# Kernel tuning notes

Hardware: AMD Instinct MI355X
Metric: run time of the kernel (lower is better)

Reference implementation:

```python
import jax, jax.numpy as jnp
import numpy as np

B, T, M, E, H = 8, 1024, 8192, 1024, 128
DECAY = 0.01
LQ_ADD = 1e-4
POS_TABLE_SIZE = 32


def setup_inputs() -> dict:
    key = jax.random.key(0)
    ks = jax.random.split(key, 9)
    return {
        "block_pos_list": jax.random.randint(ks[0], (B,), 0, 10),
        "inp": jax.random.normal(ks[1], (B, T, E), jnp.float32),
        "memory": jax.random.normal(ks[2], (B, M, E), jnp.float32),
        "memory_block_dist": jax.random.randint(ks[3], (B, M), 0, 1000).astype(jnp.int32),
        "memory_rank": jax.random.normal(ks[4], (B, M), jnp.float32),
        "pos_table": jax.random.normal(ks[5], (POS_TABLE_SIZE, E), jnp.float32) * 0.02,
        "Wk": jax.random.normal(ks[6], (H, E), jnp.float32) / np.float32(np.sqrt(E)),
        "Wq": jax.random.normal(ks[7], (H, E), jnp.float32) / np.float32(np.sqrt(E)),
        "Wv": jax.random.normal(ks[8], (H, E), jnp.float32) / np.float32(np.sqrt(E)),
    }


def reference(block_pos_list, inp, memory, memory_block_dist, memory_rank, pos_table, Wk, Wq, Wv):
    # --- reset slots where block_pos == 0 (start of a new work) ---
    reset = (block_pos_list == 0)                               # [B]
    memory = jnp.where(reset[:, None, None], 0.0, memory)       # [B, M, E]
    dist = jnp.where(reset[:, None], 0, memory_block_dist) + 1  # [B, M]

    # --- log2-bucketed positional embedding added to memory ---
    m_pos_ix = jnp.floor(jnp.log2(dist.astype(jnp.float32))).astype(jnp.int32)
    m_with_emb = memory + pos_table[m_pos_ix]                   # [B, M, E]
    mk = jnp.concatenate([m_with_emb, inp], axis=1)             # [B, M+T, E]

    # --- projections (torch Linear: x @ W.T) ---
    k = jnp.einsum('bse,he->bsh', mk, Wk)                       # [B, M+T, H]
    q = jnp.einsum('bte,he->bth', inp, Wq)                      # [B, T, H]
    v = jnp.einsum('bse,he->bsh', mk, Wv)                       # [B, M+T, H]

    # --- square + max-normalize attention (not softmax) ---
    mbs = M + T
    wei = jnp.einsum('bth,bsh->bts', q, k) * np.float32(mbs ** -0.5)  # [B, T, M+T]
    wei = wei * wei
    wei = wei / jnp.max(wei, axis=2, keepdims=True)

    # --- per-slot rank update ---
    mean_wei = jnp.mean(jnp.sum(wei, axis=1), axis=1)           # [B]
    new_rank = memory_rank + jnp.sum(wei[:, :, :M], axis=1) / mean_wei[:, None] - 1.0 - DECAY

    # --- sort memory slots by rank (descending), evict bottom block ---
    order = jnp.argsort(-new_rank, axis=1)                      # [B, M]
    mem_s = jnp.take_along_axis(memory, order[:, :, None], axis=1)
    dist_s = jnp.take_along_axis(dist, order, axis=1)
    rank_s = jnp.take_along_axis(new_rank, order, axis=1)
    r = min(T, M)
    new_memory = jax.lax.stop_gradient(mem_s.at[:, -r:].set(inp[:, -r:]))
    new_dist = dist_s.at[:, -r:].set(0)
    new_rank_out = jax.lax.stop_gradient(rank_s.at[:, -r:].set(1.0))

    qt_loss = jnp.sum(jnp.log(wei + LQ_ADD))
    out = jnp.einsum('bts,bsh->bth', wei, v)                    # [B, T, H]
    return out, qt_loss, new_memory, new_dist, new_rank_out
```

## Files before the change

### kernel.cpp

```cpp
#include <hip/hip_runtime.h>
#include <hip/hip_bf16.h>
#include <stdint.h>

#define BB 8
#define TT 1024
#define MM 8192
#define EE 1024
#define HH 128
#define SS (MM + TT)
#define RKEEP (MM - 1024)
#define NSPLIT 8
#define SCHUNK (SS / NSPLIT)
#define NT (SCHUNK / 64)
#define BK 32

typedef __attribute__((ext_vector_type(8))) short bf16x8;
typedef __attribute__((ext_vector_type(4))) short s16x4;
typedef __attribute__((ext_vector_type(4))) float f32x4;

static __device__ __forceinline__ unsigned f2ord(float f) {
    unsigned u = __float_as_uint(f);
    return u ^ ((u & 0x80000000u) ? 0xFFFFFFFFu : 0x80000000u);
}
static __device__ __forceinline__ float ord2f(unsigned o) {
    unsigned u = (o & 0x80000000u) ? (o ^ 0x80000000u) : ~o;
    return __uint_as_float(u);
}
static __device__ __forceinline__ unsigned short f2bf(float x) {
    unsigned u = __float_as_uint(x);
    unsigned r = u + 0x7FFFu + ((u >> 16) & 1u);
    return (unsigned short)(r >> 16);
}

static __device__ __forceinline__ void gload_lds16(const short* g, short* l) {
    __builtin_amdgcn_global_load_lds(
        (const __attribute__((address_space(1))) void*)g,
        (__attribute__((address_space(3))) void*)l, 16, 0, 0);
}

__device__ const float SCALEF = (float)(1.0 / 96.0);

__global__ __launch_bounds__(256) void k_wsplit(
    const float* __restrict__ Wk, const float* __restrict__ Wq, const float* __restrict__ Wv,
    short* __restrict__ wk, short* __restrict__ wq, short* __restrict__ wv)
{
    int idx = blockIdx.x * 256 + threadIdx.x;
    int m = idx >> 15;
    int o4 = (idx & 32767) * 4;
    const float* W = m == 0 ? Wk : (m == 1 ? Wq : Wv);
    short* D = m == 0 ? wk : (m == 1 ? wq : wv);
    f32x4 v = *(const f32x4*)&W[o4];
    s16x4 h;
#pragma unroll
    for (int j = 0; j < 4; ++j) h[j] = (short)f2bf(v[j]);
    *(s16x4*)&D[o4] = h;
}

__global__ __launch_bounds__(256, 4) void k_proj_kv(
    const float* __restrict__ memory, const int* __restrict__ mbd,
    const int* __restrict__ bpl, const float* __restrict__ pos_table,
    const float* __restrict__ inp,
    const short* __restrict__ wk, const short* __restrict__ wv,
    short* __restrict__ kb, short* __restrict__ vT)
{
    __shared__ __align__(16) short smA[64 * 64];
    __shared__ __align__(16) short smB[2][2][128 * 32];

    const int tid = threadIdx.x;
    const int b   = blockIdx.y;
    const int s0  = blockIdx.x * 64;
    const bool reset = (bpl[b] == 0);
    const int lane = tid & 63, wid = tid >> 6;
    const int wc = wid;
    const int fr = lane & 15, fq = lane >> 4;

    const int arow = tid >> 2;
    const int aq   = tid & 3;
    int pix;
    const float* abase;
    {
        int s = s0 + arow;
        if (s < MM) {
            int d = reset ? 1 : (mbd[b * MM + s] + 1);
            pix = 31 - __clz(d);
            abase = reset ? nullptr : &memory[((size_t)b * MM + s) * EE];
        } else {
            pix = -1;
            abase = &inp[((size_t)b * TT + (s - MM)) * EE];
        }
    }

    f32x4 accK[4][2], accV[4][2];
#pragma unroll
    for (int m = 0; m < 4; ++m)
#pragma unroll
        for (int n = 0; n < 2; ++n) {
            accK[m][n] = (f32x4){0.f, 0.f, 0.f, 0.f};
            accV[m][n] = (f32x4){0.f, 0.f, 0.f, 0.f};
        }

    const int wh   = (tid >> 2);
    const int wk8  = (tid & 3) * 8;
    const int wdst = wid * 512;

    auto STAGEW = [&](int e0, int buf) {
#pragma unroll
        for (int p = 0; p < 2; ++p) {
            int h = p * 64 + wh;
            int ec = wk8 ^ ((h & 3) << 3);
            size_t g = (size_t)h * EE + e0 + ec;
            gload_lds16(&wk[g], &smB[buf][0][p * 2048 + wdst]);
            gload_lds16(&wv[g], &smB[buf][1][p * 2048 + wdst]);
        }
    };
    auto LOADP = [&](int p, f32x4 xa[4]) {
        int e0 = p * 64 + aq * 16;
#pragma unroll
        for (int j = 0; j < 4; ++j) {
            f32x4 v = (f32x4){0.f, 0.f, 0.f, 0.f};
            if (abase) v = *(const f32x4*)&abase[e0 + j * 4];
            if (pix >= 0) {
                f32x4 pt = *(const f32x4*)&pos_table[(size_t)pix * EE + e0 + j * 4];
                v[0] += pt[0]; v[1] += pt[1]; v[2] += pt[2]; v[3] += pt[3];
            }
            xa[j] = v;
        }
    };
    auto STOREP = [&](const f32x4 xa[4]) {
#pragma unroll
        for (int j = 0; j < 2; ++j) {
            bf16x8 h;
#pragma unroll
            for (int c = 0; c < 4; ++c) {
                h[c]     = (short)f2bf(xa[2 * j][c]);
                h[4 + c] = (short)f2bf(xa[2 * j + 1][c]);
            }
            int g = (aq * 2 + j) ^ (arow & 7);
            *(bf16x8*)&smA[arow * 64 + g * 8] = h;
        }
    };

    f32x4 xa[4];
    LOADP(0, xa);
    STOREP(xa);
    STAGEW(0, 0);
    __syncthreads();
    LOADP(1, xa);

    for (int step = 0; step < 32; ++step) {
        const int wbuf = step & 1;
        const int sseg = step & 1;
        if (step < 31) STAGEW((step + 1) * BK, wbuf ^ 1);

        bf16x8 ah[4];
#pragma unroll
        for (int m = 0; m < 4; ++m) {
            int r = m * 16 + fr;
            int g = (sseg * 4 + fq) ^ (r & 7);
            ah[m] = *(const bf16x8*)&smA[r * 64 + g * 8];
        }
#pragma unroll
        for (int n = 0; n < 2; ++n) {
            int c = wc * 32 + n * 16 + fr;
            int off = c * 32 + ((fq * 8) ^ ((c & 3) << 3));
            bf16x8 kh = *(const bf16x8*)&smB[wbuf][0][off];
            bf16x8 vh = *(const bf16x8*)&smB[wbuf][1][off];
#pragma unroll
            for (int m = 0; m < 4; ++m) {
                accK[m][n] = __builtin_amdgcn_mfma_f32_16x16x32_bf16(ah[m], kh, accK[m][n], 0, 0, 0);
                accV[m][n] = __builtin_amdgcn_mfma_f32_16x16x32_bf16(ah[m], vh, accV[m][n], 0, 0, 0);
            }
        }
        __syncthreads();
        if (sseg == 1 && step < 31) {
            STOREP(xa);
            __syncthreads();
            if (step < 29) LOADP((step >> 1) + 2, xa);
        }
    }

#pragma unroll
    for (int m = 0; m < 4; ++m) {
        int row = s0 + m * 16 + fq * 4;
#pragma unroll
        for (int n = 0; n < 2; ++n) {
            int col = wc * 32 + n * 16 + fr;
#pragma unroll
            for (int i = 0; i < 4; ++i)
                kb[((size_t)b * SS + row + i) * HH + col] = (short)f2bf(accK[m][n][i]);
        }
    }
    float* tpT = (float*)smB;
#pragma unroll
    for (int hp = 0; hp < 4; ++hp) {
        __syncthreads();
        if (wc == hp) {
#pragma unroll
            for (int m = 0; m < 4; ++m)
#pragma unroll
                for (int n = 0; n < 2; ++n) {
                    int cl = n * 16 + fr;
                    int row = m * 16 + fq * 4;
                    *(f32x4*)&tpT[cl * 68 + row] = accV[m][n];
                }
        }
        __syncthreads();
        for (int idx = tid; idx < 32 * 16; idx += 256) {
            int hcl = idx >> 4, s4 = (idx & 15) << 2;
            f32x4 v = *(const f32x4*)&tpT[hcl * 68 + s4];
            s16x4 hi;
#pragma unroll
            for (int j = 0; j < 4; ++j) hi[j] = (short)f2bf(v[j]);
            size_t o = ((size_t)b * HH + hp * 32 + hcl) * SS + s0 + s4;
            *(s16x4*)&vT[o] = hi;
        }
    }
}

__global__ __launch_bounds__(256, 4) void k_proj_q(
    const float* __restrict__ inp, const short* __restrict__ wq,
    short* __restrict__ qb)
{
    __shared__ __align__(16) short smA[64 * 64];
    __shared__ __align__(16) short smB[2][128 * 32];
    const int tid = threadIdx.x;
    const int b   = blockIdx.y;
    const int t0  = blockIdx.x * 64;
    const int lane = tid & 63, wid = tid >> 6;
    const int wc = wid;
    const int fr = lane & 15, fq = lane >> 4;
    const int arow = tid >> 2, aq = tid & 3;
    const int wh   = (tid >> 2);
    const int wk8  = (tid & 3) * 8;
    const int wdst = wid * 512;
    const float* abase = &inp[((size_t)b * TT + t0 + arow) * EE];

    f32x4 acc[4][2];
#pragma unroll
    for (int m = 0; m < 4; ++m)
#pragma unroll
        for (int n = 0; n < 2; ++n) acc[m][n] = (f32x4){0.f, 0.f, 0.f, 0.f};

    auto STAGEWQ = [&](int e0, int buf) {
#pragma unroll
        for (int p = 0; p < 2; ++p) {
            int h = p * 64 + wh;
            int ec = wk8 ^ ((h & 3) << 3);
            size_t g = (size_t)h * EE + e0 + ec;
            gload_lds16(&wq[g], &smB[buf][p * 2048 + wdst]);
        }
    };
    auto LOADP = [&](int p, f32x4 xa[4]) {
        int e0 = p * 64 + aq * 16;
#pragma unroll
        for (int j = 0; j < 4; ++j) xa[j] = *(const f32x4*)&abase[e0 + j * 4];
    };
    auto STOREP = [&](const f32x4 xa[4]) {
#pragma unroll
        for (int j = 0; j < 2; ++j) {
            bf16x8 h;
#pragma unroll
            for (int c = 0; c < 4; ++c) {
                h[c]     = (short)f2bf(xa[2 * j][c]);
                h[4 + c] = (short)f2bf(xa[2 * j + 1][c]);
            }
            int g = (aq * 2 + j) ^ (arow & 7);
            *(bf16x8*)&smA[arow * 64 + g * 8] = h;
        }
    };

    f32x4 xa[4];
    LOADP(0, xa);
    STOREP(xa);
    STAGEWQ(0, 0);
    __syncthreads();
    LOADP(1, xa);

    for (int step = 0; step < 32; ++step) {
        const int wbuf = step & 1;
        const int sseg = step & 1;
        if (step < 31) STAGEWQ((step + 1) * BK, wbuf ^ 1);

        bf16x8 ah[4];
#pragma unroll
        for (int m = 0; m < 4; ++m) {
            int r = m * 16 + fr;
            int g = (sseg * 4 + fq) ^ (r & 7);
            ah[m] = *(const bf16x8*)&smA[r * 64 + g * 8];
        }
#pragma unroll
        for (int n = 0; n < 2; ++n) {
            int c = wc * 32 + n * 16 + fr;
            int off = c * 32 + ((fq * 8) ^ ((c & 3) << 3));
            bf16x8 bh = *(const bf16x8*)&smB[wbuf][off];
#pragma unroll
            for (int m = 0; m < 4; ++m)
                acc[m][n] = __builtin_amdgcn_mfma_f32_16x16x32_bf16(ah[m], bh, acc[m][n], 0, 0, 0);
        }
        __syncthreads();
        if (sseg == 1 && step < 31) {
            STOREP(xa);
            __syncthreads();
            if (step < 29) LOADP((step >> 1) + 2, xa);
        }
    }
#pragma unroll
    for (int m = 0; m < 4; ++m) {
        int row = t0 + m * 16 + fq * 4;
#pragma unroll
        for (int n = 0; n < 2; ++n) {
            int col = wc * 32 + n * 16 + fr;
#pragma unroll
            for (int i = 0; i < 4; ++i)
                qb[((size_t)b * TT + row + i) * HH + col] = (short)f2bf(acc[m][n][i]);
        }
    }
}

__device__ __forceinline__ void stage_k64_async(const short* __restrict__ src,
                                                size_t rowBase, int tid, short* sh)
{
#pragma unroll
    for (int c2 = 0; c2 < 4; ++c2) {
        int srow = c2 * 16 + (tid >> 4);
        int scol = ((tid & 15) * 8) ^ ((srow & 7) << 3);
        size_t g = (rowBase + srow) * HH + scol;
        gload_lds16(&src[g], &sh[c2 * 2048 + (tid >> 6) * 512]);
    }
}

__device__ __forceinline__ void stage_v64_async(const short* __restrict__ vT,
                                                int b, int st, int tid, short* vs)
{
#pragma unroll
    for (int c2 = 0; c2 < 4; ++c2) {
        int h = c2 * 32 + (tid >> 3);
        int sc = ((tid & 7) * 8) ^ ((h & 7) << 3);
        size_t g = ((size_t)b * HH + h) * SS + st + sc;
        gload_lds16(&vT[g], &vs[c2 * 2048 + (tid >> 6) * 512]);
    }
}

__device__ __forceinline__ void load_qfrags(const short* __restrict__ qb,
                                            size_t rowIx, int fq, bf16x8 qh[4])
{
    size_t base = rowIx * HH + fq * 8;
#pragma unroll
    for (int k = 0; k < 4; ++k)
        qh[k] = *(const bf16x8*)&qb[base + k * 32];
}

__device__ __forceinline__ void qk_mfma4(const bf16x8 qh[4], const short* sh,
                                         int fr, int fq, f32x4 acc[4])
{
#pragma unroll
    for (int n = 0; n < 4; ++n) {
        int sc = n * 16 + fr;
        int ro = sc * 128, msk = (sc & 7) << 3;
#pragma unroll
        for (int k = 0; k < 4; ++k) {
            int off = ro + ((k * 32 + fq * 8) ^ msk);
            bf16x8 bh = *(const bf16x8*)&sh[off];
            acc[n] = __builtin_amdgcn_mfma_f32_16x16x32_bf16(qh[k], bh, acc[n], 0, 0, 0);
        }
    }
}

__global__ __launch_bounds__(256) void k_rowmax(
    const short* __restrict__ qb, const short* __restrict__ kb,
    float* __restrict__ rowmax)
{
    __shared__ short Ks[2][64 * 128];
    const int tid = threadIdx.x, lane = tid & 63, wloc = tid >> 6;
    const int fr = lane & 15, fq = lane >> 4;
    const int split = blockIdx.x, t0 = blockIdx.y * 64, b = blockIdx.z;

    bf16x8 qh[4];
    load_qfrags(qb, (size_t)b * TT + t0 + wloc * 16 + fr, fq, qh);

    float rm[4] = {0.f, 0.f, 0.f, 0.f};
    const int sBeg = split * SCHUNK;
    const size_t kbase = (size_t)b * SS;

    stage_k64_async(kb, kbase + sBeg, tid, Ks[0]);
    __syncthreads();
    for (int t = 0; t < NT; ++t) {
        const int bf = t & 1;
        if (t + 1 < NT)
            stage_k64_async(kb, kbase + sBeg + (t + 1) * 64, tid, Ks[bf ^ 1]);
        f32x4 acc[4];
#pragma unroll
        for (int n = 0; n < 4; ++n) acc[n] = (f32x4){0.f, 0.f, 0.f, 0.f};
        qk_mfma4(qh, Ks[bf], fr, fq, acc);
#pragma unroll
        for (int n = 0; n < 4; ++n)
#pragma unroll
            for (int i = 0; i < 4; ++i) {
                float w = acc[n][i] * SCALEF;
                rm[i] = fmaxf(rm[i], w * w);
            }
        __syncthreads();
    }
#pragma unroll
    for (int d = 1; d < 16; d <<= 1)
#pragma unroll
        for (int i = 0; i < 4; ++i)
            rm[i] = fmaxf(rm[i], __shfl_xor(rm[i], d, 64));
    if (fr == 0)
#pragma unroll
        for (int i = 0; i < 4; ++i)
            atomicMax((int*)&rowmax[b * TT + t0 + wloc * 16 + fq * 4 + i], __float_as_int(rm[i]));
}

__global__ __launch_bounds__(256) void k_attn(
    const short* __restrict__ qb, const short* __restrict__ kb,
    const short* __restrict__ vT,
    const float* __restrict__ rowmax,
    float* __restrict__ outAcc, float* __restrict__ cpart, float* __restrict__ qtloss)
{
    __shared__ short Ks[2][64 * 128];
    __shared__ short Vs[2][128 * 64];
    __shared__ short Ph[64 * 64];
    __shared__ float csLDS[SCHUNK];
    __shared__ float qred[256];
    const int tid = threadIdx.x, lane = tid & 63, wloc = tid >> 6;
    const int fr = lane & 15, fq = lane >> 4;
    const int split = blockIdx.x, t0 = blockIdx.y * 64, b = blockIdx.z;

    for (int i = tid; i < SCHUNK; i += 256) csLDS[i] = 0.f;

    bf16x8 qh[4];
    load_qfrags(qb, (size_t)b * TT + t0 + wloc * 16 + fr, fq, qh);

    float inv[4];
#pragma unroll
    for (int i = 0; i < 4; ++i)
        inv[i] = 1.0f / rowmax[b * TT + t0 + wloc * 16 + fq * 4 + i];

    f32x4 oacc[8];
#pragma unroll
    for (int n = 0; n < 8; ++n) oacc[n] = (f32x4){0.f, 0.f, 0.f, 0.f};
    float qtp = 0.f;

    const int sBeg = split * SCHUNK;
    const size_t kbase = (size_t)b * SS;

    stage_k64_async(kb, kbase + sBeg, tid, Ks[0]);
    stage_v64_async(vT, b, sBeg, tid, Vs[0]);

    for (int t = 0; t < NT; ++t) {
        const int bf = t & 1;
        __syncthreads();

        f32x4 acc[4];
#pragma unroll
        for (int n = 0; n < 4; ++n) acc[n] = (f32x4){0.f, 0.f, 0.f, 0.f};
        qk_mfma4(qh, Ks[bf], fr, fq, acc);

#pragma unroll
        for (int n = 0; n < 4; ++n) {
            float cp = 0.f;
#pragma unroll
            for (int i = 0; i < 4; ++i) {
                float w = acc[n][i] * SCALEF;
                float w2 = w * w;
                float wei = w2 * inv[i];
                qtp += __logf(wei + 1e-4f);
                cp += wei;
                int r = wloc * 16 + fq * 4 + i;
                int sw = (n * 16 + fr) ^ ((r & 7) << 3);
                Ph[r * 64 + sw] = (short)f2bf(wei);
            }
            cp += __shfl_xor(cp, 16, 64);
            cp += __shfl_xor(cp, 32, 64);
            if (fq == 0) atomicAdd(&csLDS[t * 64 + n * 16 + fr], cp);
        }
        __syncthreads();
        if (t + 1 < NT) {
            stage_k64_async(kb, kbase + sBeg + (t + 1) * 64, tid, Ks[bf ^ 1]);
            stage_v64_async(vT, b, sBeg + (t + 1) * 64, tid, Vs[bf ^ 1]);
        }
        {
            int rA = wloc * 16 + fr;
#pragma unroll
            for (int k = 0; k < 2; ++k) {
                int offA = rA * 64 + ((k * 32 + fq * 8) ^ ((rA & 7) << 3));
                bf16x8 ph = *(const bf16x8*)&Ph[offA];
#pragma unroll
                for (int n = 0; n < 8; ++n) {
                    int hc = n * 16 + fr;
                    int offB = hc * 64 + ((k * 32 + fq * 8) ^ ((hc & 7) << 3));
                    bf16x8 vh = *(const bf16x8*)&Vs[bf][offB];
                    oacc[n] = __builtin_amdgcn_mfma_f32_16x16x32_bf16(ph, vh, oacc[n], 0, 0, 0);
                }
            }
        }
    }

#pragma unroll
    for (int n = 0; n < 8; ++n)
#pragma unroll
        for (int i = 0; i < 4; ++i)
            atomicAdd(&outAcc[((size_t)b * TT + t0 + wloc * 16 + fq * 4 + i) * HH + n * 16 + fr],
                      oacc[n][i]);

    qred[tid] = qtp;
    __syncthreads();
    for (int off = 128; off; off >>= 1) {
        if (tid < off) qred[tid] += qred[tid + off];
        __syncthreads();
    }
    if (tid == 0) atomicAdd(qtloss, qred[0]);

    const int tt = blockIdx.y;
    for (int s = tid; s < SCHUNK; s += 256)
        cpart[((size_t)(b * 16 + tt)) * SS + sBeg + s] = csLDS[s];
}

__global__ __launch_bounds__(256) void k_rank(
    const float* __restrict__ cpart, const float* __restrict__ mrank,
    unsigned long long* __restrict__ keys, float* __restrict__ csum)
{
    const int b = blockIdx.x, tid = threadIdx.x;
    __shared__ float red[256];
    float p = 0.f;
    for (int s = tid; s < SS; s += 256) {
        float cs = 0.f;
#pragma unroll
        for (int tt = 0; tt < 16; ++tt) cs += cpart[((size_t)(b * 16 + tt)) * SS + s];
        csum[b * SS + s] = cs;
        p += cs;
    }
    red[tid] = p;
    __syncthreads();
    for (int off = 128; off; off >>= 1) {
        if (tid < off) red[tid] += red[tid + off];
        __syncthreads();
    }
    float mean = red[0] / (float)SS;
    for (int m = tid; m < MM; m += 256) {
        float rank = ((mrank[b * MM + m] + csum[b * SS + m] / mean) - 1.0f) - 0.01f;
        keys[b * MM + m] = ((unsigned long long)(unsigned)(~f2ord(rank)) << 32) | (unsigned)m;
    }
}

__global__ __launch_bounds__(1024) void k_sort(unsigned long long* __restrict__ keys)
{
    __shared__ unsigned long long a[MM];
    const int b = blockIdx.x, tid = threadIdx.x;
    for (int i = tid; i < MM; i += 1024) a[i] = keys[(size_t)b * MM + i];
    __syncthreads();
    for (int k = 2; k <= MM; k <<= 1) {
        for (int j = k >> 1; j > 0; j >>= 1) {
            for (int i = tid; i < MM; i += 1024) {
                int l = i ^ j;
                if (l > i) {
                    unsigned long long x = a[i], y = a[l];
                    bool up = ((i & k) == 0);
                    if ((x > y) == up) { a[i] = y; a[l] = x; }
                }
            }
            __syncthreads();
        }
    }
    for (int i = tid; i < MM; i += 1024) keys[(size_t)b * MM + i] = a[i];
}

__global__ __launch_bounds__(256) void k_scatter(
    const float* __restrict__ memory, const int* __restrict__ mbd,
    const int* __restrict__ bpl, const float* __restrict__ inp,
    const unsigned long long* __restrict__ keys,
    float* __restrict__ nmem, float* __restrict__ ndist, float* __restrict__ nrank)
{
    const int blk = blockIdx.x;
    const int b = blk >> 10;
    const int p0 = (blk & 1023) * 8;
    const bool reset = (bpl[b] == 0);
    const int tid = threadIdx.x;
    const f32x4 zero = (f32x4){0.f, 0.f, 0.f, 0.f};

    f32x4 vr[8];
    float dist[8], rankv[8];
#pragma unroll
    for (int r = 0; r < 8; ++r) {
        int p = p0 + r;
        if (p < RKEEP) {
            unsigned long long key = keys[(size_t)b * MM + p];
            int src = (int)(unsigned)(key & 0xFFFFFFFFu);
            vr[r] = reset ? zero
                          : *(const f32x4*)&memory[((size_t)b * MM + src) * EE + tid * 4];
            dist[r]  = reset ? 1.0f : (float)(mbd[b * MM + src] + 1);
            rankv[r] = ord2f(~(unsigned)(key >> 32));
        } else {
            int irow = p - RKEEP;
            vr[r] = *(const f32x4*)&inp[((size_t)b * TT + irow) * EE + tid * 4];
            dist[r] = 0.f; rankv[r] = 1.0f;
        }
    }
#pragma unroll
    for (int r = 0; r < 8; ++r) {
        int p = p0 + r;
        *(f32x4*)&nmem[((size_t)b * MM + p) * EE + tid * 4] = vr[r];
        if (tid == 0) { ndist[b * MM + p] = dist[r]; nrank[b * MM + p] = rankv[r]; }
    }
}

extern "C" void kernel_launch(void* const* d_in, const int* in_sizes, int n_in,
                              void* d_out, int out_size, void* d_ws, size_t ws_size,
                              hipStream_t stream)
{
    const int*   bpl    = (const int*)d_in[0];
    const float* inp    = (const float*)d_in[1];
    const float* memory = (const float*)d_in[2];
    const int*   mbd    = (const int*)d_in[3];
    const float* mrank  = (const float*)d_in[4];
    const float* pos    = (const float*)d_in[5];
    const float* Wk     = (const float*)d_in[6];
    const float* Wq     = (const float*)d_in[7];
    const float* Wv     = (const float*)d_in[8];

    float* out   = (float*)d_out;
    float* qtl   = out + (size_t)BB * TT * HH;
    float* nmem  = qtl + 1;
    float* ndist = nmem + (size_t)BB * MM * EE;
    float* nrank = ndist + (size_t)BB * MM;

    char* w = (char*)d_ws;
    short* qb = (short*)w; w += (size_t)BB * TT * HH * 2;
    short* kb = (short*)w; w += (size_t)BB * SS * HH * 2;
    short* vT = (short*)w; w += (size_t)BB * HH * SS * 2;
    float* rmax = (float*)w; w += (size_t)BB * TT * 4;
    float* csum = (float*)w; w += (size_t)BB * SS * 4;
    float* cpart = (float*)w; w += (size_t)BB * 16 * SS * 4;
    unsigned long long* keys = (unsigned long long*)w; w += (size_t)BB * MM * 8;
    short* wk = (short*)w; w += (size_t)HH * EE * 2;
    short* wq = (short*)w; w += (size_t)HH * EE * 2;
    short* wv = (short*)w; w += (size_t)HH * EE * 2;
    if ((size_t)(w - (char*)d_ws) > ws_size) return;

    hipMemsetAsync(d_out, 0, ((size_t)BB * TT * HH + 1) * 4, stream);
    hipMemsetAsync(rmax, 0, (size_t)BB * TT * 4, stream);

    k_wsplit <<<384, 256, 0, stream>>>(Wk, Wq, Wv, wk, wq, wv);
    k_proj_kv<<<dim3(SS / 64, BB), 256, 0, stream>>>(memory, mbd, bpl, pos, inp,
                                                     wk, wv, kb, vT);
    k_proj_q <<<dim3(TT / 64, BB), 256, 0, stream>>>(inp, wq, qb);
    k_rowmax <<<dim3(NSPLIT, TT / 64, BB), 256, 0, stream>>>(qb, kb, rmax);
    k_attn   <<<dim3(NSPLIT, TT / 64, BB), 256, 0, stream>>>(qb, kb, vT,
                                                             rmax, out, cpart, qtl);
    k_rank   <<<BB, 256, 0, stream>>>(cpart, mrank, keys, csum);
    k_sort   <<<BB, 1024, 0, stream>>>(keys);
    k_scatter<<<BB * (MM / 8), 256, 0, stream>>>(memory, mbd, bpl, inp, keys, nmem, ndist, nrank);
}
```

Measured before the change: 575.4 us.

## Deepen async load pipelines with explicit vmcnt waits and raw barriers

Replaces __syncthreads in the projection GEMM loops with explicit s_waitcnt vmcnt/lgkmcnt plus s_barrier, and double-buffers the fp32 activation prefetch registers so global loads run two phases ahead. The rowmax kernel moves to a triple-buffered K tile with one barrier per iteration, and the attention kernel issues the next K/V tile loads before computing on the current tile instead of after. The aim is to hide global-load latency and cut barrier stalls. The cost is more registers and LDS, and hand-tuned wait counts that must exactly match the number of outstanding loads per thread, or reads could race.

```diff
diff --git a/kernel.cpp b/kernel.cpp
--- a/kernel.cpp
+++ b/kernel.cpp
@@ -17,6 +17,11 @@
 typedef __attribute__((ext_vector_type(8))) short bf16x8;
 typedef __attribute__((ext_vector_type(4))) short s16x4;
 typedef __attribute__((ext_vector_type(4))) float f32x4;
+
+#define VMCNT(n) asm volatile("s_waitcnt vmcnt(" #n ")" ::: "memory")
+#define LGKM0()  asm volatile("s_waitcnt lgkmcnt(0)" ::: "memory")
+#define SBAR()   __builtin_amdgcn_s_barrier()
+#define SCB()    __builtin_amdgcn_sched_barrier(0)
 
 static __device__ __forceinline__ unsigned f2ord(float f) {
     unsigned u = __float_as_uint(f);
@@ -118,11 +123,14 @@
 #pragma unroll
         for (int j = 0; j < 4; ++j) {
             f32x4 v = (f32x4){0.f, 0.f, 0.f, 0.f};
-            if (abase) v = *(const f32x4*)&abase[e0 + j * 4];
             if (pix >= 0) {
                 f32x4 pt = *(const f32x4*)&pos_table[(size_t)pix * EE + e0 + j * 4];
                 v[0] += pt[0]; v[1] += pt[1]; v[2] += pt[2]; v[3] += pt[3];
             }
+            if (abase) {
+                f32x4 mv = *(const f32x4*)&abase[e0 + j * 4];
+                v[0] += mv[0]; v[1] += mv[1]; v[2] += mv[2]; v[3] += mv[3];
+            }
             xa[j] = v;
         }
     };
@@ -140,18 +148,23 @@
         }
     };
 
-    f32x4 xa[4];
-    LOADP(0, xa);
-    STOREP(xa);
+    f32x4 xaA[4], xaB[4];
+    LOADP(0, xaA);
+    STOREP(xaA);
     STAGEW(0, 0);
     __syncthreads();
-    LOADP(1, xa);
+    LOADP(1, xaB);
+    LOADP(2, xaA);
 
     for (int step = 0; step < 32; ++step) {
         const int wbuf = step & 1;
+        if (step < 31) STAGEW((step + 1) * BK, wbuf ^ 1);
+        if (step == 31)                      { VMCNT(0); }
+        else if ((step & 1) || step >= 28)   { VMCNT(4); }
+        else                                 { VMCNT(8); }
+        SCB(); SBAR(); SCB();
+
         const int sseg = step & 1;
-        if (step < 31) STAGEW((step + 1) * BK, wbuf ^ 1);
-
         bf16x8 ah[4];
 #pragma unroll
         for (int m = 0; m < 4; ++m) {
@@ -171,11 +184,17 @@
                 accV[m][n] = __builtin_amdgcn_mfma_f32_16x16x32_bf16(ah[m], vh, accV[m][n], 0, 0, 0);
             }
         }
-        __syncthreads();
-        if (sseg == 1 && step < 31) {
-            STOREP(xa);
-            __syncthreads();
-            if (step < 29) LOADP((step >> 1) + 2, xa);
+
+        if (step < 31) {
+            SCB(); SBAR(); SCB();
+            if (step & 1) {
+                if ((step & 2) == 0) STOREP(xaB); else STOREP(xaA);
+                LGKM0(); SCB(); SBAR(); SCB();
+                if (step <= 25) {
+                    int np = (step >> 1) + 3;
+                    if ((step & 2) == 0) LOADP(np, xaB); else LOADP(np, xaA);
+                }
+            }
         }
     }
 
@@ -269,18 +288,23 @@
         }
     };
 
-    f32x4 xa[4];
-    LOADP(0, xa);
-    STOREP(xa);
+    f32x4 xaA[4], xaB[4];
+    LOADP(0, xaA);
+    STOREP(xaA);
     STAGEWQ(0, 0);
     __syncthreads();
-    LOADP(1, xa);
+    LOADP(1, xaB);
+    LOADP(2, xaA);
 
     for (int step = 0; step < 32; ++step) {
         const int wbuf = step & 1;
+        if (step < 31) STAGEWQ((step + 1) * BK, wbuf ^ 1);
+        if (step == 31)                      { VMCNT(0); }
+        else if ((step & 1) || step >= 28)   { VMCNT(4); }
+        else                                 { VMCNT(8); }
+        SCB(); SBAR(); SCB();
+
         const int sseg = step & 1;
-        if (step < 31) STAGEWQ((step + 1) * BK, wbuf ^ 1);
-
         bf16x8 ah[4];
 #pragma unroll
         for (int m = 0; m < 4; ++m) {
@@ -297,11 +321,17 @@
             for (int m = 0; m < 4; ++m)
                 acc[m][n] = __builtin_amdgcn_mfma_f32_16x16x32_bf16(ah[m], bh, acc[m][n], 0, 0, 0);
         }
-        __syncthreads();
-        if (sseg == 1 && step < 31) {
-            STOREP(xa);
-            __syncthreads();
-            if (step < 29) LOADP((step >> 1) + 2, xa);
+
+        if (step < 31) {
+            SCB(); SBAR(); SCB();
+            if (step & 1) {
+                if ((step & 2) == 0) STOREP(xaB); else STOREP(xaA);
+                LGKM0(); SCB(); SBAR(); SCB();
+                if (step <= 25) {
+                    int np = (step >> 1) + 3;
+                    if ((step & 2) == 0) LOADP(np, xaB); else LOADP(np, xaA);
+                }
+            }
         }
     }
 #pragma unroll
@@ -370,7 +400,7 @@
     const short* __restrict__ qb, const short* __restrict__ kb,
     float* __restrict__ rowmax)
 {
-    __shared__ short Ks[2][64 * 128];
+    __shared__ short Ks[3][64 * 128];
     const int tid = threadIdx.x, lane = tid & 63, wloc = tid >> 6;
     const int fr = lane & 15, fq = lane >> 4;
     const int split = blockIdx.x, t0 = blockIdx.y * 64, b = blockIdx.z;
@@ -383,15 +413,20 @@
     const size_t kbase = (size_t)b * SS;
 
     stage_k64_async(kb, kbase + sBeg, tid, Ks[0]);
-    __syncthreads();
+    int cur = 0;
     for (int t = 0; t < NT; ++t) {
-        const int bf = t & 1;
-        if (t + 1 < NT)
-            stage_k64_async(kb, kbase + sBeg + (t + 1) * 64, tid, Ks[bf ^ 1]);
+        int nxt = cur + 1; if (nxt == 3) nxt = 0;
+        if (t + 1 < NT) {
+            stage_k64_async(kb, kbase + sBeg + (t + 1) * 64, tid, Ks[nxt]);
+            VMCNT(4);
+        } else {
+            VMCNT(0);
+        }
+        SCB(); SBAR(); SCB();
         f32x4 acc[4];
 #pragma unroll
         for (int n = 0; n < 4; ++n) acc[n] = (f32x4){0.f, 0.f, 0.f, 0.f};
-        qk_mfma4(qh, Ks[bf], fr, fq, acc);
+        qk_mfma4(qh, Ks[cur], fr, fq, acc);
 #pragma unroll
         for (int n = 0; n < 4; ++n)
 #pragma unroll
@@ -399,7 +434,7 @@
                 float w = acc[n][i] * SCALEF;
                 rm[i] = fmaxf(rm[i], w * w);
             }
-        __syncthreads();
+        cur = nxt;
     }
 #pragma unroll
     for (int d = 1; d < 16; d <<= 1)
@@ -451,6 +486,11 @@
     for (int t = 0; t < NT; ++t) {
         const int bf = t & 1;
         __syncthreads();
+
+        if (t + 1 < NT) {
+            stage_k64_async(kb, kbase + sBeg + (t + 1) * 64, tid, Ks[bf ^ 1]);
+            stage_v64_async(vT, b, sBeg + (t + 1) * 64, tid, Vs[bf ^ 1]);
+        }
 
         f32x4 acc[4];
 #pragma unroll
@@ -475,11 +515,7 @@
             cp += __shfl_xor(cp, 32, 64);
             if (fq == 0) atomicAdd(&csLDS[t * 64 + n * 16 + fr], cp);
         }
-        __syncthreads();
-        if (t + 1 < NT) {
-            stage_k64_async(kb, kbase + sBeg + (t + 1) * 64, tid, Ks[bf ^ 1]);
-            stage_v64_async(vT, b, sBeg + (t + 1) * 64, tid, Vs[bf ^ 1]);
-        }
+        LGKM0(); SCB(); SBAR(); SCB();
         {
             int rA = wloc * 16 + fr;
 #pragma unroll
```

Result: slower. 694.3 us (+20.7%).

## Replace syncthreads with fine-grained vmcnt waits to overlap async staging

Applied to the files above, without the earlier changes.

The projection kernels issue the next weight-tile async LDS load before computing the current step and wait only on the older loads through explicit vmcnt counts plus raw s_barrier, instead of full __syncthreads. The attention kernel moves its next K/V tile prefetch to the top of the loop so it overlaps the QK and softmax-like work. Occupancy hints drop from 4 to 3 blocks per CU to give the compiler more registers. The hand-counted vmcnt values and removed barriers risk data races if the count of outstanding loads differs from what is assumed.

```diff
diff --git a/kernel.cpp b/kernel.cpp
--- a/kernel.cpp
+++ b/kernel.cpp
@@ -18,6 +18,11 @@
 typedef __attribute__((ext_vector_type(4))) short s16x4;
 typedef __attribute__((ext_vector_type(4))) float f32x4;
 
+#define VMCNT(n) asm volatile("s_waitcnt vmcnt(" #n ")" ::: "memory")
+#define LGKM0()  asm volatile("s_waitcnt lgkmcnt(0)" ::: "memory")
+#define SBAR()   __builtin_amdgcn_s_barrier()
+#define SCB()    __builtin_amdgcn_sched_barrier(0)
+
 static __device__ __forceinline__ unsigned f2ord(float f) {
     unsigned u = __float_as_uint(f);
     return u ^ ((u & 0x80000000u) ? 0xFFFFFFFFu : 0x80000000u);
@@ -56,7 +61,7 @@
     *(s16x4*)&D[o4] = h;
 }
 
-__global__ __launch_bounds__(256, 4) void k_proj_kv(
+__global__ __launch_bounds__(256, 3) void k_proj_kv(
     const float* __restrict__ memory, const int* __restrict__ mbd,
     const int* __restrict__ bpl, const float* __restrict__ pos_table,
     const float* __restrict__ inp,
@@ -149,9 +154,13 @@
 
     for (int step = 0; step < 32; ++step) {
         const int wbuf = step & 1;
+        if (step < 31) STAGEW((step + 1) * BK, wbuf ^ 1);
+        if (step == 31)                      { VMCNT(0); }
+        else if ((step & 1) || step >= 28)   { VMCNT(4); }
+        else                                 { VMCNT(8); }
+        SBAR(); SCB();
+
         const int sseg = step & 1;
-        if (step < 31) STAGEW((step + 1) * BK, wbuf ^ 1);
-
         bf16x8 ah[4];
 #pragma unroll
         for (int m = 0; m < 4; ++m) {
@@ -171,11 +180,14 @@
                 accV[m][n] = __builtin_amdgcn_mfma_f32_16x16x32_bf16(ah[m], vh, accV[m][n], 0, 0, 0);
             }
         }
-        __syncthreads();
-        if (sseg == 1 && step < 31) {
-            STOREP(xa);
-            __syncthreads();
-            if (step < 29) LOADP((step >> 1) + 2, xa);
+
+        if (step < 31) {
+            SBAR(); SCB();
+            if (step & 1) {
+                STOREP(xa);
+                LGKM0(); SBAR(); SCB();
+                if (step < 29) LOADP((step >> 1) + 2, xa);
+            }
         }
     }
 
@@ -217,7 +229,7 @@
     }
 }
 
-__global__ __launch_bounds__(256, 4) void k_proj_q(
+__global__ __launch_bounds__(256, 3) void k_proj_q(
     const float* __restrict__ inp, const short* __restrict__ wq,
     short* __restrict__ qb)
 {
@@ -278,9 +290,13 @@
 
     for (int step = 0; step < 32; ++step) {
         const int wbuf = step & 1;
+        if (step < 31) STAGEWQ((step + 1) * BK, wbuf ^ 1);
+        if (step == 31)                      { VMCNT(0); }
+        else if ((step & 1) || step >= 28)   { VMCNT(2); }
+        else                                 { VMCNT(4); }
+        SBAR(); SCB();
+
         const int sseg = step & 1;
-        if (step < 31) STAGEWQ((step + 1) * BK, wbuf ^ 1);
-
         bf16x8 ah[4];
 #pragma unroll
         for (int m = 0; m < 4; ++m) {
@@ -297,11 +313,14 @@
             for (int m = 0; m < 4; ++m)
                 acc[m][n] = __builtin_amdgcn_mfma_f32_16x16x32_bf16(ah[m], bh, acc[m][n], 0, 0, 0);
         }
-        __syncthreads();
-        if (sseg == 1 && step < 31) {
-            STOREP(xa);
-            __syncthreads();
-            if (step < 29) LOADP((step >> 1) + 2, xa);
+
+        if (step < 31) {
+            SBAR(); SCB();
+            if (step & 1) {
+                STOREP(xa);
+                LGKM0(); SBAR(); SCB();
+                if (step < 29) LOADP((step >> 1) + 2, xa);
+            }
         }
     }
 #pragma unroll
@@ -451,6 +470,11 @@
     for (int t = 0; t < NT; ++t) {
         const int bf = t & 1;
         __syncthreads();
+
+        if (t + 1 < NT) {
+            stage_k64_async(kb, kbase + sBeg + (t + 1) * 64, tid, Ks[bf ^ 1]);
+            stage_v64_async(vT, b, sBeg + (t + 1) * 64, tid, Vs[bf ^ 1]);
+        }
 
         f32x4 acc[4];
 #pragma unroll
@@ -475,11 +499,7 @@
             cp += __shfl_xor(cp, 32, 64);
             if (fq == 0) atomicAdd(&csLDS[t * 64 + n * 16 + fr], cp);
         }
-        __syncthreads();
-        if (t + 1 < NT) {
-            stage_k64_async(kb, kbase + sBeg + (t + 1) * 64, tid, Ks[bf ^ 1]);
-            stage_v64_async(vT, b, sBeg + (t + 1) * 64, tid, Vs[bf ^ 1]);
-        }
+        LGKM0(); SBAR(); SCB();
         {
             int rA = wloc * 16 + fr;
 #pragma unroll
```

Result: no change. 586.0 us (+1.8%).

## Triple-buffer weight staging and double-buffer A tiles with manual vmcnt waits

Applied to the files above, without the earlier changes.

The K/V and Q projection kernels move from double-buffered to triple-buffered weight tiles and double-buffered activation tiles. Two prefetches are kept in flight, synchronised by explicit s_waitcnt vmcnt counts and a single barrier per step instead of two __syncthreads. The attention kernel now issues the next K/V tile prefetch earlier, before the QK MFMA work, and replaces a full syncthreads with an lgkmcnt wait plus barrier. Each change is meant to overlap global loads with compute and to cut barrier stalls. In exchange, LDS use goes up, k_proj_kv drops to launch_bounds occupancy 2, and the hand-set vmcnt values must match the exact number of outstanding loads.

```diff
diff --git a/kernel.cpp b/kernel.cpp
--- a/kernel.cpp
+++ b/kernel.cpp
@@ -18,6 +18,11 @@
 typedef __attribute__((ext_vector_type(4))) short s16x4;
 typedef __attribute__((ext_vector_type(4))) float f32x4;
 
+#define VMCNT(n) asm volatile("s_waitcnt vmcnt(" #n ")" ::: "memory")
+#define LGKM0()  asm volatile("s_waitcnt lgkmcnt(0)" ::: "memory")
+#define SBAR()   __builtin_amdgcn_s_barrier()
+#define SCB()    __builtin_amdgcn_sched_barrier(0)
+
 static __device__ __forceinline__ unsigned f2ord(float f) {
     unsigned u = __float_as_uint(f);
     return u ^ ((u & 0x80000000u) ? 0xFFFFFFFFu : 0x80000000u);
@@ -56,15 +61,15 @@
     *(s16x4*)&D[o4] = h;
 }
 
-__global__ __launch_bounds__(256, 4) void k_proj_kv(
+__global__ __launch_bounds__(256, 2) void k_proj_kv(
     const float* __restrict__ memory, const int* __restrict__ mbd,
     const int* __restrict__ bpl, const float* __restrict__ pos_table,
     const float* __restrict__ inp,
     const short* __restrict__ wk, const short* __restrict__ wv,
     short* __restrict__ kb, short* __restrict__ vT)
 {
-    __shared__ __align__(16) short smA[64 * 64];
-    __shared__ __align__(16) short smB[2][2][128 * 32];
+    __shared__ __align__(16) short smA[2][64 * 64];
+    __shared__ __align__(16) short smB[3][2][128 * 32];
 
     const int tid = threadIdx.x;
     const int b   = blockIdx.y;
@@ -126,7 +131,7 @@
             xa[j] = v;
         }
     };
-    auto STOREP = [&](const f32x4 xa[4]) {
+    auto STOREP = [&](const f32x4 xa[4], int abuf) {
 #pragma unroll
         for (int j = 0; j < 2; ++j) {
             bf16x8 h;
@@ -136,28 +141,33 @@
                 h[4 + c] = (short)f2bf(xa[2 * j + 1][c]);
             }
             int g = (aq * 2 + j) ^ (arow & 7);
-            *(bf16x8*)&smA[arow * 64 + g * 8] = h;
+            *(bf16x8*)&smA[abuf][arow * 64 + g * 8] = h;
         }
     };
 
     f32x4 xa[4];
     LOADP(0, xa);
-    STOREP(xa);
+    STOREP(xa, 0);
     STAGEW(0, 0);
+    STAGEW(BK, 1);
     __syncthreads();
     LOADP(1, xa);
 
     for (int step = 0; step < 32; ++step) {
-        const int wbuf = step & 1;
-        const int sseg = step & 1;
-        if (step < 31) STAGEW((step + 1) * BK, wbuf ^ 1);
-
+        if (step == 31)                        { VMCNT(0); }
+        else if ((step & 1) || step == 30)     { VMCNT(4); }
+        else                                   { VMCNT(8); }
+        SBAR(); SCB();
+        if (step <= 29) STAGEW((step + 2) * BK, (step + 2) % 3);
+
+        const int wbuf = step % 3;
+        const int pbuf = (step >> 1) & 1;
         bf16x8 ah[4];
 #pragma unroll
         for (int m = 0; m < 4; ++m) {
             int r = m * 16 + fr;
-            int g = (sseg * 4 + fq) ^ (r & 7);
-            ah[m] = *(const bf16x8*)&smA[r * 64 + g * 8];
+            int g = (((step & 1) * 4) + fq) ^ (r & 7);
+            ah[m] = *(const bf16x8*)&smA[pbuf][r * 64 + g * 8];
         }
 #pragma unroll
         for (int n = 0; n < 2; ++n) {
@@ -171,10 +181,10 @@
                 accV[m][n] = __builtin_amdgcn_mfma_f32_16x16x32_bf16(ah[m], vh, accV[m][n], 0, 0, 0);
             }
         }
-        __syncthreads();
-        if (sseg == 1 && step < 31) {
-            STOREP(xa);
-            __syncthreads();
+
+        if ((step & 1) && step < 31) {
+            STOREP(xa, pbuf ^ 1);
+            LGKM0();
             if (step < 29) LOADP((step >> 1) + 2, xa);
         }
     }
@@ -221,8 +231,8 @@
     const float* __restrict__ inp, const short* __restrict__ wq,
     short* __restrict__ qb)
 {
-    __shared__ __align__(16) short smA[64 * 64];
-    __shared__ __align__(16) short smB[2][128 * 32];
+    __shared__ __align__(16) short smA[2][64 * 64];
+    __shared__ __align__(16) short smB[3][128 * 32];
     const int tid = threadIdx.x;
     const int b   = blockIdx.y;
     const int t0  = blockIdx.x * 64;
@@ -255,7 +265,7 @@
 #pragma unroll
         for (int j = 0; j < 4; ++j) xa[j] = *(const f32x4*)&abase[e0 + j * 4];
     };
-    auto STOREP = [&](const f32x4 xa[4]) {
+    auto STOREP = [&](const f32x4 xa[4], int abuf) {
 #pragma unroll
         for (int j = 0; j < 2; ++j) {
             bf16x8 h;
@@ -265,28 +275,33 @@
                 h[4 + c] = (short)f2bf(xa[2 * j + 1][c]);
             }
             int g = (aq * 2 + j) ^ (arow & 7);
-            *(bf16x8*)&smA[arow * 64 + g * 8] = h;
+            *(bf16x8*)&smA[abuf][arow * 64 + g * 8] = h;
         }
     };
 
     f32x4 xa[4];
     LOADP(0, xa);
-    STOREP(xa);
+    STOREP(xa, 0);
     STAGEWQ(0, 0);
+    STAGEWQ(BK, 1);
     __syncthreads();
     LOADP(1, xa);
 
     for (int step = 0; step < 32; ++step) {
-        const int wbuf = step & 1;
-        const int sseg = step & 1;
-        if (step < 31) STAGEWQ((step + 1) * BK, wbuf ^ 1);
-
+        if (step == 31)                        { VMCNT(0); }
+        else if ((step & 1) || step == 30)     { VMCNT(2); }
+        else                                   { VMCNT(6); }
+        SBAR(); SCB();
+        if (step <= 29) STAGEWQ((step + 2) * BK, (step + 2) % 3);
+
+        const int wbuf = step % 3;
+        const int pbuf = (step >> 1) & 1;
         bf16x8 ah[4];
 #pragma unroll
         for (int m = 0; m < 4; ++m) {
             int r = m * 16 + fr;
-            int g = (sseg * 4 + fq) ^ (r & 7);
-            ah[m] = *(const bf16x8*)&smA[r * 64 + g * 8];
+            int g = (((step & 1) * 4) + fq) ^ (r & 7);
+            ah[m] = *(const bf16x8*)&smA[pbuf][r * 64 + g * 8];
         }
 #pragma unroll
         for (int n = 0; n < 2; ++n) {
@@ -297,10 +312,10 @@
             for (int m = 0; m < 4; ++m)
                 acc[m][n] = __builtin_amdgcn_mfma_f32_16x16x32_bf16(ah[m], bh, acc[m][n], 0, 0, 0);
         }
-        __syncthreads();
-        if (sseg == 1 && step < 31) {
-            STOREP(xa);
-            __syncthreads();
+
+        if ((step & 1) && step < 31) {
+            STOREP(xa, pbuf ^ 1);
+            LGKM0();
             if (step < 29) LOADP((step >> 1) + 2, xa);
         }
     }
@@ -451,6 +466,11 @@
     for (int t = 0; t < NT; ++t) {
         const int bf = t & 1;
         __syncthreads();
+
+        if (t + 1 < NT) {
+            stage_k64_async(kb, kbase + sBeg + (t + 1) * 64, tid, Ks[bf ^ 1]);
+            stage_v64_async(vT, b, sBeg + (t + 1) * 64, tid, Vs[bf ^ 1]);
+        }
 
         f32x4 acc[4];
 #pragma unroll
@@ -475,11 +495,7 @@
             cp += __shfl_xor(cp, 32, 64);
             if (fq == 0) atomicAdd(&csLDS[t * 64 + n * 16 + fr], cp);
         }
-        __syncthreads();
-        if (t + 1 < NT) {
-            stage_k64_async(kb, kbase + sBeg + (t + 1) * 64, tid, Ks[bf ^ 1]);
-            stage_v64_async(vT, b, sBeg + (t + 1) * 64, tid, Vs[bf ^ 1]);
-        }
+        LGKM0(); SBAR(); SCB();
         {
             int rA = wloc * 16 + fr;
 #pragma unroll
```

New measurement: 597.4 us. 1.04x slower.
